# Kernel optimization log

Hardware: AMD Instinct MI355X
Metric: run time of the kernel (lower is better)

Reference implementation:

```python
import jax, jax.numpy as jnp
import numpy as np

# ---- static config (mirrors DRR.__init__ kwargs) ----
NX = NY = NZ = 192            # volume dims
H = W = 192                   # detector height/width
SDR = 300.0                   # source-to-rotation-center distance
DELX = DELY = 2.0             # detector pixel pitch (mm)
X0 = Y0 = 0.0                 # detector offsets
SPACING = (1.0, 1.0, 1.0)     # voxel spacing (mm)
BAM = 1.0                     # bone_attenuation_multiplier
B = 2                         # batch (poses)
N_SUB = H * W // 2            # p_subsample = 0.5


def setup_inputs() -> dict:
    key = jax.random.key(0)
    k1, k2, k3, k4 = jax.random.split(key, 4)
    # CT volume in Hounsfield units, spanning air (-1000) to bone (~2000)
    volume = jax.random.uniform(k1, (NX, NY, NZ), jnp.float32, -1000.0, 2000.0)
    rotations = jax.random.normal(k2, (B, 3), jnp.float32)          # Euler ZYX (rad)
    translations = jax.random.normal(k3, (B, 3), jnp.float32) * 10.0  # mm, near isocenter
    # unique subsampled detector pixel indices (Detector.subsamples[-1])
    subsample_idx = jax.random.permutation(k4, H * W)[:N_SUB].astype(jnp.int32)
    return {"volume": volume, "rotations": rotations,
            "translations": translations, "subsample_idx": subsample_idx}


def _rz(t):
    c, s = jnp.cos(t), jnp.sin(t); z = jnp.zeros_like(t); o = jnp.ones_like(t)
    return jnp.stack([jnp.stack([c, -s, z], -1),
                      jnp.stack([s, c, z], -1),
                      jnp.stack([z, z, o], -1)], -2)


def _ry(t):
    c, s = jnp.cos(t), jnp.sin(t); z = jnp.zeros_like(t); o = jnp.ones_like(t)
    return jnp.stack([jnp.stack([c, z, s], -1),
                      jnp.stack([z, o, z], -1),
                      jnp.stack([-s, z, c], -1)], -2)


def _rx(t):
    c, s = jnp.cos(t), jnp.sin(t); z = jnp.zeros_like(t); o = jnp.ones_like(t)
    return jnp.stack([jnp.stack([o, z, z], -1),
                      jnp.stack([z, c, -s], -1),
                      jnp.stack([z, s, c], -1)], -2)


def _density(volume):
    # DRR.__init__: volume.flip([0]); air/soft/bone HU segmentation + normalization
    vol = jnp.flip(volume, 0)
    soft = (vol > -800.0) & (vol <= 350.0)
    soft_min = jnp.min(jnp.where(soft, vol, jnp.inf))
    d = jnp.where(vol <= -800.0, soft_min,
                  jnp.where(vol > 350.0, vol * BAM, vol))
    d = d - jnp.min(d)
    return d / jnp.max(d)


def _canonical_detector():
    # source on +z at SDR, detector plane at -z; pixel grid with pitch delx/dely
    xs = (jnp.arange(W, dtype=jnp.float32) - (W - 1) / 2.0) * DELX + X0
    ys = (jnp.arange(H, dtype=jnp.float32) - (H - 1) / 2.0) * DELY + Y0
    gy, gx = jnp.meshgrid(ys, xs, indexing="ij")
    tgt = jnp.stack([gx.ravel(), gy.ravel(),
                     jnp.full((H * W,), -SDR, jnp.float32)], -1)  # [H*W, 3]
    src = jnp.array([0.0, 0.0, SDR], jnp.float32)
    return src, tgt


def _siddon(density, source, target):
    """Siddon ray-casting. source [B,3], target [B,N,3] -> line integrals [B,N]."""
    dims = density.shape
    sp = jnp.asarray(SPACING, density.dtype)
    src = source[:, None, :]                     # [B,1,3]
    sdd = target - src                           # [B,N,3]
    sdd_safe = jnp.where(sdd == 0, 1e-9, sdd)
    # parametric intersections with all grid planes per axis
    alist = [(jnp.arange(dims[a] + 1, dtype=density.dtype)[None, None, :] * sp[a]
              - src[..., a:a + 1]) / sdd_safe[..., a:a + 1] for a in range(3)]
    a_first = jnp.stack([al[..., 0] for al in alist], -1)    # [B,N,3]
    a_last = jnp.stack([al[..., -1] for al in alist], -1)
    amin = jnp.maximum(jnp.max(jnp.minimum(a_first, a_last), -1), 0.0)[..., None]
    amax = jnp.minimum(jnp.min(jnp.maximum(a_first, a_last), -1), 1.0)[..., None]
    amax = jnp.maximum(amax, amin)               # ray misses -> zero-length segments
    alphas = jnp.sort(jnp.clip(jnp.concatenate(alist, -1), amin, amax), -1)  # [B,N,M+1]
    mid = 0.5 * (alphas[..., 1:] + alphas[..., :-1])                         # [B,N,M]
    ray_len = jnp.linalg.norm(target - src, axis=-1, keepdims=True)
    step = (alphas[..., 1:] - alphas[..., :-1]) * ray_len                    # [B,N,M]
    pts = src[..., None, :] + mid[..., None] * sdd[..., None, :]             # [B,N,M,3]
    idx = jnp.clip(jnp.floor(pts / sp).astype(jnp.int32), 0,
                   jnp.array(dims, jnp.int32) - 1)
    vox = density[idx[..., 0], idx[..., 1], idx[..., 2]]                     # gather
    return jnp.sum(step * vox, -1)


def reference(volume, rotations, translations, subsample_idx):
    density = _density(volume)
    src_c, tgt_c = _canonical_detector()
    tgt_c = tgt_c[subsample_idx]                                  # [N,3] subsampled rays
    R = _rz(rotations[:, 0]) @ _ry(rotations[:, 1]) @ _rx(rotations[:, 2])  # [B,3,3]
    center = jnp.array([NX, NY, NZ], jnp.float32) * jnp.asarray(SPACING, jnp.float32) / 2.0
    t = translations + center                                     # pose about isocenter
    source = jnp.einsum("bij,j->bi", R, src_c) + t                # [B,3]
    target = jnp.einsum("bij,nj->bni", R, tgt_c) + t[:, None, :]  # [B,N,3]
    img = _siddon(density, source, target)                        # [B,N]
    # reshape_subsampled_drr: scatter into zeros [B, H*W] then view [B,1,H,W]
    drr = jnp.zeros((img.shape[0], H * W), img.dtype).at[:, subsample_idx].set(img)
    return drr.reshape(-1, 1, H, W)
```

## Files before the change

kernel.cpp:

```cpp
#include <hip/hip_runtime.h>
#include <float.h>
#include <math.h>


#define NDIM   192
#define HW     (NDIM * NDIM)
#define NSUB   (HW / 2)
#define NTILE  576
#define NBATCH 2
#define NCHUNK 16
#define NVOX   (NDIM * NDIM * NDIM)
#define SDRF   300.0f
#define RBLK   1728

#define WS_LIST_OFF 16
#define WS_PART_OFF (WS_LIST_OFF + 4 * NSUB)

__global__ __launch_bounds__(256) void reduce_kernel(
    const float* __restrict__ vol, float* __restrict__ parts) {
    const int tid = blockIdx.x * 256 + threadIdx.x;
    const float4* __restrict__ v4 = (const float4*)vol;
    const int S = RBLK * 256;

    float4 r0 = v4[tid + 0 * S];
    float4 r1 = v4[tid + 1 * S];
    float4 r2 = v4[tid + 2 * S];
    float4 r3 = v4[tid + 3 * S];

    float smin = FLT_MAX, rmin = FLT_MAX, rmax = -FLT_MAX;
    float4 rr[4] = {r0, r1, r2, r3};
#pragma unroll
    for (int k = 0; k < 4; ++k) {
        float xs[4] = {rr[k].x, rr[k].y, rr[k].z, rr[k].w};
#pragma unroll
        for (int j = 0; j < 4; ++j) {
            float x = xs[j];
            bool in = (x > -800.0f);
            rmin = fminf(rmin, in ? x : FLT_MAX);
            rmax = fmaxf(rmax, in ? x : -FLT_MAX);
            smin = fminf(smin, (in && x <= 350.0f) ? x : FLT_MAX);
        }
    }
#pragma unroll
    for (int off = 32; off > 0; off >>= 1) {
        smin = fminf(smin, __shfl_down(smin, off));
        rmin = fminf(rmin, __shfl_down(rmin, off));
        rmax = fmaxf(rmax, __shfl_down(rmax, off));
    }
    __shared__ float sm[4], rm[4], rx[4];
    int w = threadIdx.x >> 6;
    if ((threadIdx.x & 63) == 0) { sm[w] = smin; rm[w] = rmin; rx[w] = rmax; }
    __syncthreads();
    if (threadIdx.x == 0) {
        parts[blockIdx.x] =
            fminf(fminf(sm[0], sm[1]), fminf(sm[2], sm[3]));
        parts[RBLK + blockIdx.x] =
            fminf(fminf(rm[0], rm[1]), fminf(rm[2], rm[3]));
        parts[2 * RBLK + blockIdx.x] =
            fmaxf(fmaxf(rx[0], rx[1]), fmaxf(rx[2], rx[3]));
    }
}

__device__ __forceinline__ int key_to_pixel(int tile, int lane) {
    int pi = (tile / 24) * 8 + (lane >> 3);
    int pj = (tile % 24) * 8 + (lane & 7);
    return pi * NDIM + pj;
}

__global__ __launch_bounds__(1024) void setup_kernel(
    const float* __restrict__ parts, const int* __restrict__ sidx,
    float* __restrict__ wsf, int* __restrict__ list) {
    __shared__ unsigned char smark[HW];
    __shared__ int s[NTILE];
    __shared__ float sm[16], rm[16], rx[16];
    const int t = threadIdx.x;

    int4* sm4 = (int4*)smark;
    for (int i = t; i < HW / 16; i += 1024) sm4[i] = make_int4(0, 0, 0, 0);

    float smin = FLT_MAX, rmin = FLT_MAX, rmax = -FLT_MAX;
    for (int i = t; i < RBLK; i += 1024) {
        smin = fminf(smin, parts[i]);
        rmin = fminf(rmin, parts[RBLK + i]);
        rmax = fmaxf(rmax, parts[2 * RBLK + i]);
    }
#pragma unroll
    for (int off = 32; off > 0; off >>= 1) {
        smin = fminf(smin, __shfl_down(smin, off));
        rmin = fminf(rmin, __shfl_down(rmin, off));
        rmax = fmaxf(rmax, __shfl_down(rmax, off));
    }
    int w = t >> 6;
    if ((t & 63) == 0) { sm[w] = smin; rm[w] = rmin; rx[w] = rmax; }
    __syncthreads();

    for (int i = t; i < NSUB; i += 1024) smark[sidx[i]] = 1;
    if (t == 0) {
        float a = FLT_MAX, b = FLT_MAX, c = -FLT_MAX;
#pragma unroll
        for (int k = 0; k < 16; ++k) {
            a = fminf(a, sm[k]); b = fminf(b, rm[k]); c = fmaxf(c, rx[k]);
        }
        wsf[0] = a; wsf[1] = b; wsf[2] = c;
    }
    __syncthreads();

    int cnt = 0;
    if (t < NTILE) {
#pragma unroll 8
        for (int lane = 0; lane < 64; ++lane)
            cnt += smark[key_to_pixel(t, lane)];
        s[t] = cnt;
    }
    __syncthreads();
    for (int off = 1; off < NTILE; off <<= 1) {
        int v = 0, u = 0;
        if (t < NTILE) {
            v = s[t];
            u = (t >= off) ? s[t - off] : 0;
        }
        __syncthreads();
        if (t < NTILE) s[t] = v + u;
        __syncthreads();
    }
    if (t < NTILE) {
        int pos = s[t] - cnt;
        for (int lane = 0; lane < 64; ++lane) {
            int p = key_to_pixel(t, lane);
            if (smark[p]) list[pos++] = p;
        }
    }
}

__device__ __forceinline__ void init_axis(float s, float d, float a_lo,
                                          int& i, int& st, float& na) {
    if (d > 0.0f) {
        st = 1;
        float f = s + a_lo * d;
        int ii = (int)floorf(f) + 1;
        ii = max(0, min(ii, NDIM + 1));
        while (ii <= NDIM && ((float)ii - s) / d <= a_lo) ++ii;
        while (ii > 0 && ((float)(ii - 1) - s) / d > a_lo) --ii;
        i  = ii;
        na = (ii <= NDIM) ? ((float)ii - s) / d : FLT_MAX;
    } else {
        st = -1;
        float f = s + a_lo * d;
        int ii = (int)ceilf(f) - 1;
        ii = max(-1, min(ii, NDIM));
        while (ii >= 0 && ((float)ii - s) / d <= a_lo) --ii;
        while (ii < NDIM && ((float)(ii + 1) - s) / d > a_lo) ++ii;
        i  = ii;
        na = (ii >= 0) ? ((float)ii - s) / d : FLT_MAX;
    }
}

__global__ __launch_bounds__(256) void ray_kernel(
    const float* __restrict__ vol, const float* __restrict__ rot,
    const float* __restrict__ trans, const float* __restrict__ wsc,
    const int* __restrict__ list, float* __restrict__ out) {
    const int n = blockIdx.x * 256 + threadIdx.x;
    const int c = blockIdx.y;
    const int b = blockIdx.z;

    const int p  = list[n];
    const int pi = p / NDIM;
    const int pj = p % NDIM;

    float smin = wsc[0];
    float rmin = wsc[1];
    float rmax = wsc[2];
    float dmin = fminf(smin, rmin);
    float dmax = fmaxf(smin, rmax);
    float scale = 1.0f / (dmax - dmin);

    float rz = rot[b * 3 + 0], ry = rot[b * 3 + 1], rx = rot[b * 3 + 2];
    float cz = cosf(rz), sz = sinf(rz);
    float cy = cosf(ry), sy = sinf(ry);
    float cx = cosf(rx), sx = sinf(rx);
    float R00 = cz * cy;
    float R01 = cz * sy * sx - sz * cx;
    float R02 = sz * sx + cz * sy * cx;
    float R10 = sz * cy;
    float R11 = cz * cx + sz * sy * sx;
    float R12 = sz * sy * cx - cz * sx;
    float R20 = -sy;
    float R21 = cy * sx;
    float R22 = cy * cx;
    float tx = trans[b * 3 + 0] + 96.0f;
    float ty = trans[b * 3 + 1] + 96.0f;
    float tz = trans[b * 3 + 2] + 96.0f;

    float srcx = R02 * SDRF + tx;
    float srcy = R12 * SDRF + ty;
    float srcz = R22 * SDRF + tz;
    float gx = ((float)pj - 95.5f) * 2.0f;
    float gy = ((float)pi - 95.5f) * 2.0f;
    float tgx = R00 * gx + R01 * gy + R02 * (-SDRF) + tx;
    float tgy = R10 * gx + R11 * gy + R12 * (-SDRF) + ty;
    float tgz = R20 * gx + R21 * gy + R22 * (-SDRF) + tz;

    float sdx = tgx - srcx, sdy = tgy - srcy, sdz = tgz - srcz;
    float dsx = (sdx == 0.0f) ? 1e-9f : sdx;
    float dsy = (sdy == 0.0f) ? 1e-9f : sdy;
    float dsz = (sdz == 0.0f) ? 1e-9f : sdz;

    float af0 = (0.0f - srcx) / dsx, al0 = (192.0f - srcx) / dsx;
    float af1 = (0.0f - srcy) / dsy, al1 = (192.0f - srcy) / dsy;
    float af2 = (0.0f - srcz) / dsz, al2 = (192.0f - srcz) / dsz;
    float amin = fmaxf(fmaxf(fminf(af0, al0), fminf(af1, al1)), fminf(af2, al2));
    amin = fmaxf(amin, 0.0f);
    float amax = fminf(fminf(fmaxf(af0, al0), fmaxf(af1, al1)), fmaxf(af2, al2));
    amax = fminf(amax, 1.0f);
    amax = fmaxf(amax, amin);
    float ray_len = sqrtf(sdx * sdx + sdy * sdy + sdz * sdz);

    float span = amax - amin;
    float a_lo = amin + span * ((float)c / (float)NCHUNK);
    float a_hi = (c == NCHUNK - 1) ? amax
                                   : amin + span * ((float)(c + 1) / (float)NCHUNK);

    int i0, i1, i2, st0, st1, st2;
    float na0, na1, na2;
    init_axis(srcx, dsx, a_lo, i0, st0, na0);
    init_axis(srcy, dsy, a_lo, i1, st1, na1);
    init_axis(srcz, dsz, a_lo, i2, st2, na2);

    float r0 = 1.0f / dsx, r1 = 1.0f / dsy, r2 = 1.0f / dsz;
    float fi0 = (float)i0, fi1 = (float)i1, fi2 = (float)i2;
    float fs0 = (float)st0, fs1 = (float)st1, fs2 = (float)st2;

    float cur = a_lo;
    float acc = 0.0f;
    bool fin = false;
    while (!fin) {
        float an  = fminf(fminf(na0, na1), na2);
        fin = !(an < a_hi);
        float a2  = fin ? a_hi : an;
        float mid = 0.5f * (cur + a2);
        float px = fmaf(mid, sdx, srcx);
        float py = fmaf(mid, sdy, srcy);
        float pz = fmaf(mid, sdz, srcz);
        int ix = min(max((int)px, 0), NDIM - 1);
        int iy = min(max((int)py, 0), NDIM - 1);
        int iz = min(max((int)pz, 0), NDIM - 1);
        int addr = (NDIM - 1) * HW - ix * HW + iy * NDIM + iz;
        float v  = vol[addr];
        bool c0 = (na0 == an), c1 = (na1 == an), c2 = (na2 == an);
        float nf0 = fi0 + fs0, nf1 = fi1 + fs1, nf2 = fi2 + fs2;
        float nn0 = (nf0 - srcx) * r0;
        float nn1 = (nf1 - srcy) * r1;
        float nn2 = (nf2 - srcz) * r2;
        fi0 = c0 ? nf0 : fi0;  na0 = c0 ? nn0 : na0;
        fi1 = c1 ? nf1 : fi1;  na1 = c1 ? nn1 : na1;
        fi2 = c2 ? nf2 : fi2;  na2 = c2 ? nn2 : na2;
        float dv = (v <= -800.0f) ? smin : v;
        acc = fmaf(a2 - cur, dv, acc);
        cur = a2;
    }
    float res = (acc - dmin * (a_hi - a_lo)) * scale * ray_len;
    atomicAdd(&out[b * HW + p], res);
}

extern "C" void kernel_launch(void* const* d_in, const int* in_sizes, int n_in,
                              void* d_out, int out_size, void* d_ws,
                              size_t ws_size, hipStream_t stream) {
    const float* vol   = (const float*)d_in[0];
    const float* rot   = (const float*)d_in[1];
    const float* trans = (const float*)d_in[2];
    const int*   sidx  = (const int*)d_in[3];
    float* out = (float*)d_out;

    float* wsf   = (float*)d_ws;
    int*   list  = (int*)((unsigned char*)d_ws + WS_LIST_OFF);
    float* parts = (float*)((unsigned char*)d_ws + WS_PART_OFF);

    hipMemsetAsync(d_out, 0, (size_t)out_size * sizeof(float), stream);
    reduce_kernel<<<RBLK, 256, 0, stream>>>(vol, parts);
    setup_kernel<<<1, 1024, 0, stream>>>(parts, sidx, wsf, list);
    dim3 rgrid(NSUB / 256, NCHUNK, NBATCH);
    ray_kernel<<<rgrid, 256, 0, stream>>>(vol, rot, trans, wsf, list, out);
}
```

Measured before the change: 131.5 us.

## Precompute normalized fp16 density volume and remap ray blocks across XCDs

Adds a densify pass that flips, segments and normalizes the CT volume into an fp16 array, so the ray kernel gathers 2-byte pre-normalized densities instead of raw fp32 HU values and skips the per-sample select and final affine correction. The ray grid is flattened to 1D and block indices are remapped so each XCD handles one batch and a contiguous set of pixel blocks, aiming for better L2 locality. This costs an extra full-volume read/write pass and introduces fp16 rounding in the accumulated line integrals.

New measurement: 141.5 us. 1.08x slower.

```diff
diff --git a/kernel.cpp b/kernel.cpp
--- a/kernel.cpp
+++ b/kernel.cpp
@@ -1,4 +1,5 @@
 #include <hip/hip_runtime.h>
+#include <hip/hip_fp16.h>
 #include <float.h>
 #include <math.h>
 
@@ -14,7 +15,8 @@
 #define RBLK   1728
 
 #define WS_LIST_OFF 16
-#define WS_PART_OFF (WS_LIST_OFF + 4 * NSUB)
+#define WS_PART_OFF (16 + 4 * NSUB)
+#define WS_DENS_OFF 98304
 
 __global__ __launch_bounds__(256) void reduce_kernel(
     const float* __restrict__ vol, float* __restrict__ parts) {
@@ -130,6 +132,34 @@
             if (smark[p]) list[pos++] = p;
         }
     }
+}
+
+__global__ __launch_bounds__(256) void densify_kernel(
+    const float* __restrict__ vol, const float* __restrict__ wsf,
+    __half* __restrict__ dens) {
+    const int t = blockIdx.x * 256 + threadIdx.x;
+    const int o = t * 16;
+    const int ox = o / HW;
+    const int rem = o - ox * HW;
+
+    float smin = wsf[0];
+    float dmin = fminf(smin, wsf[1]);
+    float scale = 1.0f / (fmaxf(smin, wsf[2]) - dmin);
+
+    const float4* s4 = (const float4*)(vol + (NDIM - 1 - ox) * HW + rem);
+    float4 a0 = s4[0], a1 = s4[1], a2 = s4[2], a3 = s4[3];
+    float xs[16] = {a0.x, a0.y, a0.z, a0.w, a1.x, a1.y, a1.z, a1.w,
+                    a2.x, a2.y, a2.z, a2.w, a3.x, a3.y, a3.z, a3.w};
+    union { __half h[16]; int4 q[2]; } u;
+#pragma unroll
+    for (int k = 0; k < 16; ++k) {
+        float v = xs[k];
+        float d = (v <= -800.0f) ? smin : v;
+        u.h[k] = __float2half_rn((d - dmin) * scale);
+    }
+    int4* d4 = (int4*)(dens + o);
+    d4[0] = u.q[0];
+    d4[1] = u.q[1];
 }
 
 __device__ __forceinline__ void init_axis(float s, float d, float a_lo,
@@ -156,23 +186,21 @@
 }
 
 __global__ __launch_bounds__(256) void ray_kernel(
-    const float* __restrict__ vol, const float* __restrict__ rot,
-    const float* __restrict__ trans, const float* __restrict__ wsc,
-    const int* __restrict__ list, float* __restrict__ out) {
-    const int n = blockIdx.x * 256 + threadIdx.x;
-    const int c = blockIdx.y;
-    const int b = blockIdx.z;
+    const __half* __restrict__ dens, const float* __restrict__ rot,
+    const float* __restrict__ trans, const int* __restrict__ list,
+    float* __restrict__ out) {
+    const int bid = blockIdx.x;
+    const int xcd  = bid & 7;
+    const int s_   = bid >> 3;
+    const int b    = xcd >> 2;
+    const int xr   = xcd & 3;
+    const int c    = s_ & 15;
+    const int pblk = s_ >> 4;
+    const int n = (xr * 18 + pblk) * 256 + threadIdx.x;
 
     const int p  = list[n];
     const int pi = p / NDIM;
     const int pj = p % NDIM;
-
-    float smin = wsc[0];
-    float rmin = wsc[1];
-    float rmax = wsc[2];
-    float dmin = fminf(smin, rmin);
-    float dmax = fmaxf(smin, rmax);
-    float scale = 1.0f / (dmax - dmin);
 
     float rz = rot[b * 3 + 0], ry = rot[b * 3 + 1], rx = rot[b * 3 + 2];
     float cz = cosf(rz), sz = sinf(rz);
@@ -244,8 +272,8 @@
         int ix = min(max((int)px, 0), NDIM - 1);
         int iy = min(max((int)py, 0), NDIM - 1);
         int iz = min(max((int)pz, 0), NDIM - 1);
-        int addr = (NDIM - 1) * HW - ix * HW + iy * NDIM + iz;
-        float v  = vol[addr];
+        int addr = ix * HW + iy * NDIM + iz;
+        float dv = __half2float(dens[addr]);
         bool c0 = (na0 == an), c1 = (na1 == an), c2 = (na2 == an);
         float nf0 = fi0 + fs0, nf1 = fi1 + fs1, nf2 = fi2 + fs2;
         float nn0 = (nf0 - srcx) * r0;
@@ -254,12 +282,10 @@
         fi0 = c0 ? nf0 : fi0;  na0 = c0 ? nn0 : na0;
         fi1 = c1 ? nf1 : fi1;  na1 = c1 ? nn1 : na1;
         fi2 = c2 ? nf2 : fi2;  na2 = c2 ? nn2 : na2;
-        float dv = (v <= -800.0f) ? smin : v;
         acc = fmaf(a2 - cur, dv, acc);
         cur = a2;
     }
-    float res = (acc - dmin * (a_hi - a_lo)) * scale * ray_len;
-    atomicAdd(&out[b * HW + p], res);
+    atomicAdd(&out[b * HW + p], acc * ray_len);
 }
 
 extern "C" void kernel_launch(void* const* d_in, const int* in_sizes, int n_in,
@@ -271,13 +297,15 @@
     const int*   sidx  = (const int*)d_in[3];
     float* out = (float*)d_out;
 
-    float* wsf   = (float*)d_ws;
-    int*   list  = (int*)((unsigned char*)d_ws + WS_LIST_OFF);
-    float* parts = (float*)((unsigned char*)d_ws + WS_PART_OFF);
+    float*  wsf   = (float*)d_ws;
+    int*    list  = (int*)((unsigned char*)d_ws + WS_LIST_OFF);
+    float*  parts = (float*)((unsigned char*)d_ws + WS_PART_OFF);
+    __half* dens  = (__half*)((unsigned char*)d_ws + WS_DENS_OFF);
 
     hipMemsetAsync(d_out, 0, (size_t)out_size * sizeof(float), stream);
     reduce_kernel<<<RBLK, 256, 0, stream>>>(vol, parts);
     setup_kernel<<<1, 1024, 0, stream>>>(parts, sidx, wsf, list);
-    dim3 rgrid(NSUB / 256, NCHUNK, NBATCH);
-    ray_kernel<<<rgrid, 256, 0, stream>>>(vol, rot, trans, wsf, list, out);
-}
+    densify_kernel<<<RBLK, 256, 0, stream>>>(vol, wsf, dens);
+    ray_kernel<<<NCHUNK * NBATCH * (NSUB / 256), 256, 0, stream>>>(
+        dens, rot, trans, list, out);
+}
```

## Pick pose-aware pixel tiling, XCD-aware block mapping, and software-pipeline ray loop

Applied to the files above, without the earlier changes.

Setup now builds two ordered pixel lists with differently shaped 4x16 and 16x4 tiles. Each ray block picks the list whose long tile axis matches how the rotated detector lines up with the volume's fastest axis, so neighbouring lanes should gather nearby voxels. The ray grid is flattened and remapped so each of the 8 XCDs gets a fixed batch and pixel range, which is meant to keep voxel reuse inside one L2. The traversal loop is also unrolled by two so the next voxel load is issued before the current one is accumulated, hiding gather latency at the cost of more registers and extra serial scan work in setup.

New measurement: 146.5 us. 1.11x slower.

```diff
diff --git a/kernel.cpp b/kernel.cpp
--- a/kernel.cpp
+++ b/kernel.cpp
@@ -13,8 +13,9 @@
 #define SDRF   300.0f
 #define RBLK   1728
 
-#define WS_LIST_OFF 16
-#define WS_PART_OFF (WS_LIST_OFF + 4 * NSUB)
+#define WS_LISTA_OFF 16
+#define WS_LISTB_OFF (WS_LISTA_OFF + 4 * NSUB)
+#define WS_PART_OFF  (WS_LISTB_OFF + 4 * NSUB)
 
 __global__ __launch_bounds__(256) void reduce_kernel(
     const float* __restrict__ vol, float* __restrict__ parts) {
@@ -61,15 +62,21 @@
     }
 }
 
-__device__ __forceinline__ int key_to_pixel(int tile, int lane) {
-    int pi = (tile / 24) * 8 + (lane >> 3);
-    int pj = (tile % 24) * 8 + (lane & 7);
+__device__ __forceinline__ int keyA(int tile, int lane) {
+    int pi = (tile / 12) * 4 + (lane >> 4);
+    int pj = (tile % 12) * 16 + (lane & 15);
+    return pi * NDIM + pj;
+}
+__device__ __forceinline__ int keyB(int tile, int lane) {
+    int pi = (tile / 48) * 16 + (lane & 15);
+    int pj = (tile % 48) * 4 + (lane >> 4);
     return pi * NDIM + pj;
 }
 
 __global__ __launch_bounds__(1024) void setup_kernel(
     const float* __restrict__ parts, const int* __restrict__ sidx,
-    float* __restrict__ wsf, int* __restrict__ list) {
+    float* __restrict__ wsf, int* __restrict__ listA,
+    int* __restrict__ listB) {
     __shared__ unsigned char smark[HW];
     __shared__ int s[NTILE];
     __shared__ float sm[16], rm[16], rx[16];
@@ -108,17 +115,13 @@
     int cnt = 0;
     if (t < NTILE) {
 #pragma unroll 8
-        for (int lane = 0; lane < 64; ++lane)
-            cnt += smark[key_to_pixel(t, lane)];
+        for (int lane = 0; lane < 64; ++lane) cnt += smark[keyA(t, lane)];
         s[t] = cnt;
     }
     __syncthreads();
     for (int off = 1; off < NTILE; off <<= 1) {
         int v = 0, u = 0;
-        if (t < NTILE) {
-            v = s[t];
-            u = (t >= off) ? s[t - off] : 0;
-        }
+        if (t < NTILE) { v = s[t]; u = (t >= off) ? s[t - off] : 0; }
         __syncthreads();
         if (t < NTILE) s[t] = v + u;
         __syncthreads();
@@ -126,8 +129,31 @@
     if (t < NTILE) {
         int pos = s[t] - cnt;
         for (int lane = 0; lane < 64; ++lane) {
-            int p = key_to_pixel(t, lane);
-            if (smark[p]) list[pos++] = p;
+            int p = keyA(t, lane);
+            if (smark[p]) listA[pos++] = p;
+        }
+    }
+    __syncthreads();
+
+    cnt = 0;
+    if (t < NTILE) {
+#pragma unroll 8
+        for (int lane = 0; lane < 64; ++lane) cnt += smark[keyB(t, lane)];
+        s[t] = cnt;
+    }
+    __syncthreads();
+    for (int off = 1; off < NTILE; off <<= 1) {
+        int v = 0, u = 0;
+        if (t < NTILE) { v = s[t]; u = (t >= off) ? s[t - off] : 0; }
+        __syncthreads();
+        if (t < NTILE) s[t] = v + u;
+        __syncthreads();
+    }
+    if (t < NTILE) {
+        int pos = s[t] - cnt;
+        for (int lane = 0; lane < 64; ++lane) {
+            int p = keyB(t, lane);
+            if (smark[p]) listB[pos++] = p;
         }
     }
 }
@@ -158,21 +184,20 @@
 __global__ __launch_bounds__(256) void ray_kernel(
     const float* __restrict__ vol, const float* __restrict__ rot,
     const float* __restrict__ trans, const float* __restrict__ wsc,
-    const int* __restrict__ list, float* __restrict__ out) {
-    const int n = blockIdx.x * 256 + threadIdx.x;
-    const int c = blockIdx.y;
-    const int b = blockIdx.z;
-
-    const int p  = list[n];
-    const int pi = p / NDIM;
-    const int pj = p % NDIM;
+    const int* __restrict__ listA, const int* __restrict__ listB,
+    float* __restrict__ out) {
+    const int bid = blockIdx.x;
+    const int xcd  = bid & 7;
+    const int s_   = bid >> 3;
+    const int b    = xcd >> 2;
+    const int xr   = xcd & 3;
+    const int c    = s_ & 15;
+    const int pblk = s_ >> 4;
+    const int n = (xr * 18 + pblk) * 256 + threadIdx.x;
 
     float smin = wsc[0];
-    float rmin = wsc[1];
-    float rmax = wsc[2];
-    float dmin = fminf(smin, rmin);
-    float dmax = fmaxf(smin, rmax);
-    float scale = 1.0f / (dmax - dmin);
+    float dmin = fminf(smin, wsc[1]);
+    float scale = 1.0f / (fmaxf(smin, wsc[2]) - dmin);
 
     float rz = rot[b * 3 + 0], ry = rot[b * 3 + 1], rx = rot[b * 3 + 2];
     float cz = cosf(rz), sz = sinf(rz);
@@ -187,6 +212,12 @@
     float R20 = -sy;
     float R21 = cy * sx;
     float R22 = cy * cx;
+
+    const int* __restrict__ list = (fabsf(R20) >= fabsf(R21)) ? listA : listB;
+    const int p  = list[n];
+    const int pi = p / NDIM;
+    const int pj = p % NDIM;
+
     float tx = trans[b * 3 + 0] + 96.0f;
     float ty = trans[b * 3 + 1] + 96.0f;
     float tz = trans[b * 3 + 2] + 96.0f;
@@ -232,11 +263,11 @@
 
     float cur = a_lo;
     float acc = 0.0f;
-    bool fin = false;
-    while (!fin) {
-        float an  = fminf(fminf(na0, na1), na2);
+
+    auto compute_seg = [&](float& step, bool& fin, float& v) {
+        float an = fminf(fminf(na0, na1), na2);
         fin = !(an < a_hi);
-        float a2  = fin ? a_hi : an;
+        float a2 = fin ? a_hi : an;
         float mid = 0.5f * (cur + a2);
         float px = fmaf(mid, sdx, srcx);
         float py = fmaf(mid, sdy, srcy);
@@ -244,8 +275,7 @@
         int ix = min(max((int)px, 0), NDIM - 1);
         int iy = min(max((int)py, 0), NDIM - 1);
         int iz = min(max((int)pz, 0), NDIM - 1);
-        int addr = (NDIM - 1) * HW - ix * HW + iy * NDIM + iz;
-        float v  = vol[addr];
+        v = vol[(NDIM - 1) * HW - ix * HW + iy * NDIM + iz];
         bool c0 = (na0 == an), c1 = (na1 == an), c2 = (na2 == an);
         float nf0 = fi0 + fs0, nf1 = fi1 + fs1, nf2 = fi2 + fs2;
         float nn0 = (nf0 - srcx) * r0;
@@ -254,9 +284,24 @@
         fi0 = c0 ? nf0 : fi0;  na0 = c0 ? nn0 : na0;
         fi1 = c1 ? nf1 : fi1;  na1 = c1 ? nn1 : na1;
         fi2 = c2 ? nf2 : fi2;  na2 = c2 ? nn2 : na2;
+        step = a2 - cur;
+        cur = a2;
+    };
+    auto consume = [&](float step, float v) {
         float dv = (v <= -800.0f) ? smin : v;
-        acc = fmaf(a2 - cur, dv, acc);
-        cur = a2;
+        acc = fmaf(step, dv, acc);
+    };
+
+    float stepA, stepB, vA, vB;
+    bool  finA,  finB;
+    compute_seg(stepA, finA, vA);
+    while (true) {
+        if (finA) { consume(stepA, vA); break; }
+        compute_seg(stepB, finB, vB);
+        consume(stepA, vA);
+        if (finB) { consume(stepB, vB); break; }
+        compute_seg(stepA, finA, vA);
+        consume(stepB, vB);
     }
     float res = (acc - dmin * (a_hi - a_lo)) * scale * ray_len;
     atomicAdd(&out[b * HW + p], res);
@@ -272,12 +317,13 @@
     float* out = (float*)d_out;
 
     float* wsf   = (float*)d_ws;
-    int*   list  = (int*)((unsigned char*)d_ws + WS_LIST_OFF);
+    int*   listA = (int*)((unsigned char*)d_ws + WS_LISTA_OFF);
+    int*   listB = (int*)((unsigned char*)d_ws + WS_LISTB_OFF);
     float* parts = (float*)((unsigned char*)d_ws + WS_PART_OFF);
 
     hipMemsetAsync(d_out, 0, (size_t)out_size * sizeof(float), stream);
     reduce_kernel<<<RBLK, 256, 0, stream>>>(vol, parts);
-    setup_kernel<<<1, 1024, 0, stream>>>(parts, sidx, wsf, list);
-    dim3 rgrid(NSUB / 256, NCHUNK, NBATCH);
-    ray_kernel<<<rgrid, 256, 0, stream>>>(vol, rot, trans, wsf, list, out);
-}
+    setup_kernel<<<1, 1024, 0, stream>>>(parts, sidx, wsf, listA, listB);
+    ray_kernel<<<NCHUNK * NBATCH * (NSUB / 256), 256, 0, stream>>>(
+        vol, rot, trans, wsf, listA, listB, out);
+}
```
